# Kernel tuning notes

Hardware: AMD Instinct MI355X
Metric: run time of the kernel (lower is better)

The kernel has to match this reference:

```python
import jax, jax.numpy as jnp
import numpy as np

N = 50000
E = 800000
D = 128
H = 8
HD = D // H


def setup_inputs() -> dict:
    key = jax.random.key(0)
    ks = jax.random.split(key, 12)
    s = 1.0 / np.sqrt(D)
    x = jax.random.normal(ks[0], (N, D), dtype=jnp.float32)
    edge_index = jax.random.randint(ks[1], (2, E), 0, N, dtype=jnp.int64)
    edge_bias = jax.random.normal(ks[2], (E, H), dtype=jnp.float32)
    Wq = jax.random.uniform(ks[3], (D, D), jnp.float32, -s, s)
    bq = jax.random.uniform(ks[4], (D,), jnp.float32, -s, s)
    Wk = jax.random.uniform(ks[5], (D, D), jnp.float32, -s, s)
    bk = jax.random.uniform(ks[6], (D,), jnp.float32, -s, s)
    Wv = jax.random.uniform(ks[7], (D, D), jnp.float32, -s, s)
    bv = jax.random.uniform(ks[8], (D,), jnp.float32, -s, s)
    Wo = jax.random.uniform(ks[9], (D, D), jnp.float32, -s, s)
    bo = jax.random.uniform(ks[10], (D,), jnp.float32, -s, s)
    return {"x": x, "edge_index": edge_index, "edge_bias": edge_bias,
            "Wq": Wq, "bq": bq, "Wk": Wk, "bk": bk,
            "Wv": Wv, "bv": bv, "Wo": Wo, "bo": bo}


def reference(x, edge_index, edge_bias, Wq, bq, Wk, bk, Wv, bv, Wo, bo):
    scale = HD ** -0.5
    row, col = edge_index[0], edge_index[1]
    # Node-level projections -> [N, H, HD]
    q = (x @ Wq + bq).reshape(N, H, HD)
    k = (x @ Wk + bk).reshape(N, H, HD)
    v = (x @ Wv + bv).reshape(N, H, HD)
    # Edge-level gather + per-edge attention logits [E, H]
    q_i = q[col]
    k_j = k[row]
    v_j = v[row]
    attn = jnp.einsum('ehd,ehd->eh', q_i, k_j) * scale + edge_bias
    # Scatter-softmax over incoming edges of each destination node (col)
    seg_max = jax.ops.segment_max(attn, col, num_segments=N)  # [N, H]
    seg_max = jnp.where(jnp.isfinite(seg_max), seg_max, 0.0)  # empty segments -> 0
    ex = jnp.exp(attn - seg_max[col])
    denom = jax.ops.segment_sum(ex, col, num_segments=N)      # [N, H]
    attn = ex / (denom[col] + 1e-16)
    # Scatter-add weighted values -> [N, H, HD]
    weighted_v = attn[:, :, None] * v_j
    out = jax.ops.segment_sum(weighted_v, col, num_segments=N)
    out = out.reshape(N, D)
    return out @ Wo + bo
```

## Files before the change

### kernel.cpp

```cpp
#include <hip/hip_runtime.h>
#include <math.h>

#define NN 50000
#define EE 800000
#define DD 128
#define HH 8
#define HDD 16
#define CAP 64
#define GB 391
#define PAD 136

typedef __attribute__((ext_vector_type(8))) short short8;
typedef __attribute__((ext_vector_type(4))) float f32x4;

union U8 { ushort u[8]; int4 v; short8 s; };

__device__ __forceinline__ ushort f2bf(float f) {
    uint u = __float_as_uint(f);
    uint r = (u + 0x7fffu + ((u >> 16) & 1u)) >> 16;
    return (ushort)r;
}
__device__ __forceinline__ float bf2f(ushort u) {
    return __uint_as_float(((uint)u) << 16);
}

__global__ void k_prep(const float* __restrict__ Wq, const float* __restrict__ Wk,
                       const float* __restrict__ Wv, const float* __restrict__ Wo,
                       const float* __restrict__ bq, const float* __restrict__ bk,
                       const float* __restrict__ bv, const float* __restrict__ bo,
                       ushort* __restrict__ Wt, float* __restrict__ bpack) {
    int tid = blockIdx.x * 256 + threadIdx.x;
    int w = tid >> 14, rem = tid & 16383, c = rem >> 7, i = rem & 127;
    const float* W = (w == 0) ? Wq : (w == 1) ? Wk : (w == 2) ? Wv : Wo;
    float s = (w == 0) ? 0.25f : 1.0f;
    Wt[(size_t)w * 16384 + c * 128 + i] = f2bf(W[i * 128 + c] * s);
    if (i == 0) {
        const float* B = (w == 0) ? bq : (w == 1) ? bk : (w == 2) ? bv : bo;
        bpack[w * 128 + c] = B[c] * s;
    }
}

__global__ void k_fill(const int* __restrict__ col, const int* __restrict__ row,
                       int* __restrict__ cursor, int2* __restrict__ reB) {
    int e = blockIdx.x * 256 + threadIdx.x;
    if (e >= EE) return;
    int c = col[e];
    int p = atomicAdd(&cursor[c], 1);
    if (p < CAP) reB[(size_t)c * CAP + p] = make_int2(row[e], e);
}

__global__ __launch_bounds__(256) void k_qkv3(
    const float* __restrict__ x, const ushort* __restrict__ Wt,
    const float* __restrict__ bpk,
    ushort* __restrict__ qb, ushort* __restrict__ kk, ushort* __restrict__ vv) {
    __shared__ ushort lA[128 * PAD];
    int tid = threadIdx.x;
    int lane = tid & 63, wave = tid >> 6;
    int r0 = blockIdx.x * 128;

#pragma unroll
    for (int it = 0; it < 8; it++) {
        int slot = it * 256 + tid;
        int arow = slot >> 4, c8 = slot & 15;
        int ar = min(r0 + arow, NN - 1);
        const float* xp = x + (size_t)ar * 128 + c8 * 8;
        float4 a = *(const float4*)xp;
        float4 b = *(const float4*)(xp + 4);
        U8 r;
        r.u[0] = f2bf(a.x); r.u[1] = f2bf(a.y); r.u[2] = f2bf(a.z); r.u[3] = f2bf(a.w);
        r.u[4] = f2bf(b.x); r.u[5] = f2bf(b.y); r.u[6] = f2bf(b.z); r.u[7] = f2bf(b.w);
        *(int4*)&lA[arow * PAD + c8 * 8] = r.v;
    }
    __syncthreads();

    int wm = wave >> 1, wn = wave & 1;
    int lr = lane & 15, lg = lane >> 4;

    for (int w = 0; w < 3; w++) {
        f32x4 acc[4][4];
#pragma unroll
        for (int m = 0; m < 4; m++)
#pragma unroll
            for (int n = 0; n < 4; n++) acc[m][n] = (f32x4){0.f, 0.f, 0.f, 0.f};

#pragma unroll
        for (int ks = 0; ks < 4; ks++) {
            short8 a[4], b[4];
#pragma unroll
            for (int m = 0; m < 4; m++)
                a[m] = *(const short8*)&lA[(wm * 64 + m * 16 + lr) * PAD + ks * 32 + lg * 8];
#pragma unroll
            for (int n = 0; n < 4; n++)
                b[n] = *(const short8*)&Wt[(size_t)w * 16384 +
                                           (wn * 64 + n * 16 + lr) * 128 + ks * 32 + lg * 8];
#pragma unroll
            for (int m = 0; m < 4; m++)
#pragma unroll
                for (int n = 0; n < 4; n++)
                    acc[m][n] = __builtin_amdgcn_mfma_f32_16x16x32_bf16(a[m], b[n], acc[m][n], 0, 0, 0);
        }

#pragma unroll
        for (int n = 0; n < 4; n++) {
            int gcol = wn * 64 + n * 16 + lr;
            float bv_ = bpk[w * 128 + gcol];
#pragma unroll
            for (int m = 0; m < 4; m++) {
#pragma unroll
                for (int rg = 0; rg < 4; rg++) {
                    int grow = r0 + wm * 64 + m * 16 + lg * 4 + rg;
                    if (grow < NN) {
                        float val = acc[m][n][rg] + bv_;
                        ushort h16 = f2bf(val);
                        if (w == 0)      qb[(size_t)grow * 128 + gcol] = h16;
                        else if (w == 1) kk[(size_t)grow * 128 + gcol] = h16;
                        else             vv[(size_t)grow * 128 + gcol] = h16;
                    }
                }
            }
        }
    }
}

__global__ __launch_bounds__(256) void k_gemm128(
    const ushort* __restrict__ A, const ushort* __restrict__ Bt,
    const float* __restrict__ bias, float* __restrict__ Cf, int M) {
    int tid = threadIdx.x;
    int lane = tid & 63, wave = tid >> 6;
    int r0 = blockIdx.x * 128;
    int wm = wave >> 1, wn = wave & 1;
    int lr = lane & 15, lg = lane >> 4;

    f32x4 acc[4][4];
#pragma unroll
    for (int m = 0; m < 4; m++)
#pragma unroll
        for (int n = 0; n < 4; n++) acc[m][n] = (f32x4){0.f, 0.f, 0.f, 0.f};

#pragma unroll
    for (int ks = 0; ks < 4; ks++) {
        short8 a[4], b[4];
#pragma unroll
        for (int m = 0; m < 4; m++) {
            int ar = min(r0 + wm * 64 + m * 16 + lr, M - 1);
            a[m] = *(const short8*)&A[(size_t)ar * 128 + ks * 32 + lg * 8];
        }
#pragma unroll
        for (int n = 0; n < 4; n++)
            b[n] = *(const short8*)&Bt[(wn * 64 + n * 16 + lr) * 128 + ks * 32 + lg * 8];
#pragma unroll
        for (int m = 0; m < 4; m++)
#pragma unroll
            for (int n = 0; n < 4; n++)
                acc[m][n] = __builtin_amdgcn_mfma_f32_16x16x32_bf16(a[m], b[n], acc[m][n], 0, 0, 0);
    }

#pragma unroll
    for (int n = 0; n < 4; n++) {
        int gcol = wn * 64 + n * 16 + lr;
        float bv_ = bias[gcol];
#pragma unroll
        for (int m = 0; m < 4; m++) {
#pragma unroll
            for (int rg = 0; rg < 4; rg++) {
                int grow = r0 + wm * 64 + m * 16 + lg * 4 + rg;
                if (grow < M) Cf[(size_t)grow * 128 + gcol] = acc[m][n][rg] + bv_;
            }
        }
    }
}

__global__ __launch_bounds__(256) void k_attn(
    const ushort* __restrict__ qb, const ushort* __restrict__ kk,
    const ushort* __restrict__ vv, const float* __restrict__ ebias,
    const int2* __restrict__ reB, const int* __restrict__ deg,
    ushort* __restrict__ aggb) {
    int wave = threadIdx.x >> 6;
    int lane = threadIdx.x & 63;
    int n = blockIdx.x * 4 + wave;
    if (n >= NN) return;
    int cnt = min(deg[n], CAP);
    const int2* bucket = reB + (size_t)n * CAP;
    int h = lane >> 3;
    int j = lane & 7;
    int hb = lane & ~7;

    float qf[16];
    {
        U8 q0, q1;
        const ushort* qp = qb + (size_t)n * DD + h * HDD;
        q0.v = *(const int4*)qp;
        q1.v = *(const int4*)(qp + 8);
#pragma unroll
        for (int t = 0; t < 8; t++) qf[t] = bf2f(q0.u[t]);
#pragma unroll
        for (int t = 0; t < 8; t++) qf[8 + t] = bf2f(q1.u[t]);
    }

    float m = -INFINITY;
    float denom = 0.f;
    float acc0 = 0.f, acc1 = 0.f;

    for (int idx = 0; idx < cnt; idx += 8) {
        int my = idx + j;
        bool valid = my < cnt;
        int2 re = valid ? bucket[my] : make_int2(0, 0);
        int r = re.x;
        float logit = -INFINITY;
        if (valid) {
            const ushort* kp = kk + (size_t)r * DD + h * HDD;
            U8 a0, a1;
            a0.v = *(const int4*)kp;
            a1.v = *(const int4*)(kp + 8);
            float d = 0.f;
#pragma unroll
            for (int t = 0; t < 8; t++) d += qf[t] * bf2f(a0.u[t]);
#pragma unroll
            for (int t = 0; t < 8; t++) d += qf[8 + t] * bf2f(a1.u[t]);
            logit = d + ebias[(size_t)re.y * HH + h];
        }
        float cm = logit;
        cm = fmaxf(cm, __shfl_xor(cm, 1));
        cm = fmaxf(cm, __shfl_xor(cm, 2));
        cm = fmaxf(cm, __shfl_xor(cm, 4));
        float mnew = fmaxf(m, cm);
        float sc = __expf(m - mnew);
        float p = __expf(logit - mnew);
        m = mnew;
        float ps = p;
        ps += __shfl_xor(ps, 1);
        ps += __shfl_xor(ps, 2);
        ps += __shfl_xor(ps, 4);
        denom = denom * sc + ps;
        acc0 *= sc;
        acc1 *= sc;
#pragma unroll
        for (int j2 = 0; j2 < 8; j2++) {
            float pj = __shfl(p, hb + j2);
            int rj = __shfl(r, hb + j2);
            uint vp = *(const uint*)(vv + (size_t)rj * DD + 2 * lane);
            acc0 += pj * bf2f((ushort)(vp & 0xffffu));
            acc1 += pj * bf2f((ushort)(vp >> 16));
        }
    }
    float inv = 1.0f / (denom + 1e-16f);
    uint pack = (uint)f2bf(acc0 * inv) | ((uint)f2bf(acc1 * inv) << 16);
    *(uint*)&aggb[(size_t)n * DD + 2 * lane] = pack;
}

extern "C" void kernel_launch(void* const* d_in, const int* in_sizes, int n_in,
                              void* d_out, int out_size, void* d_ws, size_t ws_size,
                              hipStream_t stream) {
    const float* x     = (const float*)d_in[0];
    const int*   eidx  = (const int*)d_in[1];
    const float* ebias = (const float*)d_in[2];
    const float* Wq    = (const float*)d_in[3];
    const float* bq    = (const float*)d_in[4];
    const float* Wk    = (const float*)d_in[5];
    const float* bk    = (const float*)d_in[6];
    const float* Wv    = (const float*)d_in[7];
    const float* bv    = (const float*)d_in[8];
    const float* Wo    = (const float*)d_in[9];
    const float* bo    = (const float*)d_in[10];
    float* out = (float*)d_out;

    const int* row = eidx;
    const int* col = eidx + EE;

    char* p = (char*)d_ws;
    ushort* qb    = (ushort*)p;  p += (size_t)NN * DD * 2;
    ushort* kk    = (ushort*)p;  p += (size_t)NN * DD * 2;
    ushort* vvp   = (ushort*)p;  p += (size_t)NN * DD * 2;
    ushort* aggb  = (ushort*)p;  p += (size_t)NN * DD * 2;
    ushort* Wt    = (ushort*)p;  p += (size_t)4 * 16384 * 2;
    float*  bpk   = (float*)p;   p += 4 * 128 * 4;
    int2*   reB   = (int2*)p;    p += (size_t)NN * CAP * 8;
    int* cursor   = (int*)p;     p += (size_t)NN * 4;

    hipMemsetAsync(cursor, 0, (size_t)NN * sizeof(int), stream);

    hipLaunchKernelGGL(k_prep, dim3(256), dim3(256), 0, stream,
                       Wq, Wk, Wv, Wo, bq, bk, bv, bo, Wt, bpk);

    hipLaunchKernelGGL(k_fill, dim3(EE / 256), dim3(256), 0, stream,
                       col, row, cursor, reB);

    hipLaunchKernelGGL(k_qkv3, dim3(GB), dim3(256), 0, stream,
                       x, Wt, bpk, qb, kk, vvp);

    hipLaunchKernelGGL(k_attn, dim3(NN / 4), dim3(256), 0, stream,
                       qb, kk, vvp, ebias, reB, cursor, aggb);

    hipLaunchKernelGGL(k_gemm128, dim3(GB), dim3(256), 0, stream,
                       aggb, Wt + 3 * 16384, bpk + 3 * 128, out, NN);
}
```

Baseline: 218.0 us.

## Fuse edge-bucket fill and QKV projection into one interleaved kernel

Merges the atomic edge-bucketing kernel and the QKV GEMM kernel into a single launch. Block indices are interleaved so every ninth block runs a GEMM tile and the other eight each bucket 256 edges. The aim is to overlap the memory- and atomic-bound fill with the MFMA-bound projection and to drop one kernel launch. The GEMM blocks still reserve the large LDS tile, and the new launch bound of 4 blocks per CU may raise register pressure in the GEMM path.

```diff
diff --git a/kernel.cpp b/kernel.cpp
--- a/kernel.cpp
+++ b/kernel.cpp
@@ -8,6 +8,7 @@
 #define HDD 16
 #define CAP 64
 #define GB 391
+#define TOTB 3519
 #define PAD 136
 
 typedef __attribute__((ext_vector_type(8))) short short8;
@@ -40,23 +41,30 @@
     }
 }
 
-__global__ void k_fill(const int* __restrict__ col, const int* __restrict__ row,
-                       int* __restrict__ cursor, int2* __restrict__ reB) {
-    int e = blockIdx.x * 256 + threadIdx.x;
-    if (e >= EE) return;
-    int c = col[e];
-    int p = atomicAdd(&cursor[c], 1);
-    if (p < CAP) reB[(size_t)c * CAP + p] = make_int2(row[e], e);
-}
-
-__global__ __launch_bounds__(256) void k_qkv3(
+__global__ __launch_bounds__(256, 4) void k_pre(
     const float* __restrict__ x, const ushort* __restrict__ Wt,
     const float* __restrict__ bpk,
-    ushort* __restrict__ qb, ushort* __restrict__ kk, ushort* __restrict__ vv) {
+    ushort* __restrict__ qb, ushort* __restrict__ kk, ushort* __restrict__ vv,
+    const int* __restrict__ col, const int* __restrict__ row,
+    int* __restrict__ cursor, int2* __restrict__ reB) {
     __shared__ ushort lA[128 * PAD];
     int tid = threadIdx.x;
+    int b = blockIdx.x;
+
+    if (b % 9 != 0) {
+        int fi = b - b / 9 - 1;
+        int e = fi * 256 + tid;
+        if (e < EE) {
+            int c = col[e];
+            int p = atomicAdd(&cursor[c], 1);
+            if (p < CAP) reB[(size_t)c * CAP + p] = make_int2(row[e], e);
+        }
+        return;
+    }
+
+    int tile = b / 9;
     int lane = tid & 63, wave = tid >> 6;
-    int r0 = blockIdx.x * 128;
+    int r0 = tile * 128;
 
 #pragma unroll
     for (int it = 0; it < 8; it++) {
@@ -65,10 +73,10 @@
         int ar = min(r0 + arow, NN - 1);
         const float* xp = x + (size_t)ar * 128 + c8 * 8;
         float4 a = *(const float4*)xp;
-        float4 b = *(const float4*)(xp + 4);
+        float4 bb = *(const float4*)(xp + 4);
         U8 r;
         r.u[0] = f2bf(a.x); r.u[1] = f2bf(a.y); r.u[2] = f2bf(a.z); r.u[3] = f2bf(a.w);
-        r.u[4] = f2bf(b.x); r.u[5] = f2bf(b.y); r.u[6] = f2bf(b.z); r.u[7] = f2bf(b.w);
+        r.u[4] = f2bf(bb.x); r.u[5] = f2bf(bb.y); r.u[6] = f2bf(bb.z); r.u[7] = f2bf(bb.w);
         *(int4*)&lA[arow * PAD + c8 * 8] = r.v;
     }
     __syncthreads();
@@ -85,19 +93,19 @@
 
 #pragma unroll
         for (int ks = 0; ks < 4; ks++) {
-            short8 a[4], b[4];
+            short8 a[4], bfr[4];
 #pragma unroll
             for (int m = 0; m < 4; m++)
                 a[m] = *(const short8*)&lA[(wm * 64 + m * 16 + lr) * PAD + ks * 32 + lg * 8];
 #pragma unroll
             for (int n = 0; n < 4; n++)
-                b[n] = *(const short8*)&Wt[(size_t)w * 16384 +
-                                           (wn * 64 + n * 16 + lr) * 128 + ks * 32 + lg * 8];
+                bfr[n] = *(const short8*)&Wt[(size_t)w * 16384 +
+                                             (wn * 64 + n * 16 + lr) * 128 + ks * 32 + lg * 8];
 #pragma unroll
             for (int m = 0; m < 4; m++)
 #pragma unroll
                 for (int n = 0; n < 4; n++)
-                    acc[m][n] = __builtin_amdgcn_mfma_f32_16x16x32_bf16(a[m], b[n], acc[m][n], 0, 0, 0);
+                    acc[m][n] = __builtin_amdgcn_mfma_f32_16x16x32_bf16(a[m], bfr[n], acc[m][n], 0, 0, 0);
         }
 
 #pragma unroll
@@ -282,11 +290,8 @@
     hipLaunchKernelGGL(k_prep, dim3(256), dim3(256), 0, stream,
                        Wq, Wk, Wv, Wo, bq, bk, bv, bo, Wt, bpk);
 
-    hipLaunchKernelGGL(k_fill, dim3(EE / 256), dim3(256), 0, stream,
-                       col, row, cursor, reB);
-
-    hipLaunchKernelGGL(k_qkv3, dim3(GB), dim3(256), 0, stream,
-                       x, Wt, bpk, qb, kk, vvp);
+    hipLaunchKernelGGL(k_pre, dim3(TOTB), dim3(256), 0, stream,
+                       x, Wt, bpk, qb, kk, vvp, col, row, cursor, reB);
 
     hipLaunchKernelGGL(k_attn, dim3(NN / 4), dim3(256), 0, stream,
                        qb, kk, vvp, ebias, reB, cursor, aggb);
```

After: 249.4 us. 1.14x slower.
